# Performance work log

Hardware: AMD Instinct MI355X
Metric: run time of the kernel (lower is better)

The kernel has to match this reference:

```python
import jax, jax.numpy as jnp
import numpy as np

B = 131072
H_DIM = 256
DT = 0.05


def setup_inputs() -> dict:
    key = jax.random.key(0)
    ks = jax.random.split(key, 20)
    w = lambda k, shape, fan_in: jax.random.normal(k, shape, jnp.float32) / np.sqrt(fan_in)
    return {
        "q": jax.random.normal(ks[0], (B, 1), jnp.float32),
        "p": jax.random.normal(ks[1], (B, 1), jnp.float32),
        "u": jax.random.normal(ks[2], (B, 1), jnp.float32),
        "Wk1": w(ks[3], (H_DIM, 2), 2), "bk1": w(ks[4], (H_DIM,), 2),
        "Wk2": w(ks[5], (H_DIM, H_DIM), H_DIM), "bk2": w(ks[6], (H_DIM,), H_DIM),
        "Wk3": w(ks[7], (1, H_DIM), H_DIM), "bk3": w(ks[8], (1,), H_DIM),
        "Wp1": w(ks[9], (H_DIM, 1), 1), "bp1": w(ks[10], (H_DIM,), 1),
        "Wp2": w(ks[11], (H_DIM, H_DIM), H_DIM), "bp2": w(ks[12], (H_DIM,), H_DIM),
        "Wp3": w(ks[13], (1, H_DIM), H_DIM), "bp3": w(ks[14], (1,), H_DIM),
        "b_ctrl": jax.random.normal(ks[15], (1, 1), jnp.float32) * 0.01,
    }


def reference(q, p, u, Wk1, bk1, Wk2, bk2, Wk3, bk3, Wp1, bp1, Wp2, bp2, Wp3, bp3, b_ctrl):
    sp = jax.nn.softplus

    def H(z):  # z: (B, 2) -> (B,)
        qz = z[:, :1]
        hk = sp(z @ Wk1.T + bk1)
        hk = sp(hk @ Wk2.T + bk2)
        T = (hk @ Wk3.T + bk3)[:, 0]
        hp = sp(qz @ Wp1.T + bp1)
        hp = sp(hp @ Wp2.T + bp2)
        V = (hp @ Wp3.T + bp3)[:, 0]
        return T + V

    grad_H = jax.grad(lambda z: H(z).sum())
    # M = J - R with R = 0, J fixed symplectic form
    M = jnp.array([[0.0, 1.0], [-1.0, 0.0]], jnp.float32)
    ctrl = jnp.concatenate([jnp.zeros_like(q), u @ b_ctrl.T], axis=-1)  # (B, 2)

    def dyn(q_, p_):
        # torch detaches z before autograd.grad -> stop_gradient matches semantics
        z = jax.lax.stop_gradient(jnp.concatenate([q_, p_], axis=-1))
        dz = grad_H(z) @ M.T + ctrl
        return dz[:, :1], dz[:, 1:]

    dt = DT
    dq1, dp1 = dyn(q, p)
    dq2, dp2 = dyn(q + 0.5 * dt * dq1, p + 0.5 * dt * dp1)
    dq3, dp3 = dyn(q + 0.5 * dt * dq2, p + 0.5 * dt * dp2)
    dq4, dp4 = dyn(q + dt * dq3, p + dt * dp3)
    q_next = q + dt / 6.0 * (dq1 + 2 * dq2 + 2 * dq3 + dq4)
    p_next = p + dt / 6.0 * (dp1 + 2 * dp2 + 2 * dp3 + dp4)
    return (q_next, p_next)
```

## Files before the change

kernel.cpp:

```cpp
#include <hip/hip_runtime.h>
#include <hip/hip_bf16.h>

#define NB   131072
#define TPB  1024
#define SPB  512

typedef __attribute__((ext_vector_type(8))) short short8;
typedef __attribute__((ext_vector_type(4))) float f32x4;
typedef __attribute__((ext_vector_type(4))) unsigned short ushort4v;

__device__ __forceinline__ unsigned short f2bf(float f) {
    union { float f; unsigned int u; } v; v.f = f;
    unsigned int r = v.u + 0x7fff + ((v.u >> 16) & 1);
    return (unsigned short)(r >> 16);
}

__device__ __forceinline__ unsigned int cvt_pk_bf16(float lo, float hi) {
    unsigned int r;
    asm("v_cvt_pk_bf16_f32 %0, %1, %2" : "=v"(r) : "v"(lo), "v"(hi));
    return r;
}
__device__ __forceinline__ float fexp2(float x) {
    float r; asm("v_exp_f32 %0, %1" : "=v"(r) : "v"(x)); return r;
}
__device__ __forceinline__ float flog2(float x) {
    float r; asm("v_log_f32 %0, %1" : "=v"(r) : "v"(x)); return r;
}

__global__ void prep_weights(const float* __restrict__ Wk2, const float* __restrict__ Wp2,
                             unsigned short* __restrict__ out) {
    int idx = blockIdx.x * blockDim.x + threadIdx.x;
    int n = idx >> 8, k = idx & 255;
    unsigned short a = f2bf(Wk2[idx]);
    out[idx] = a;
    out[65536 + k * 256 + n] = a;
    unsigned short b = f2bf(Wp2[idx]);
    out[131072 + idx] = b;
    out[196608 + k * 256 + n] = b;
}

__launch_bounds__(TPB, 4)
__global__ void phgn_main(const float* __restrict__ q_in, const float* __restrict__ p_in,
                          const float* __restrict__ u_in,
                          const float* __restrict__ Wk1, const float* __restrict__ bk1,
                          const float* __restrict__ bk2, const float* __restrict__ wk3,
                          const float* __restrict__ wp1, const float* __restrict__ bp1,
                          const float* __restrict__ bp2, const float* __restrict__ wp3,
                          const float* __restrict__ bctrl,
                          const unsigned short* __restrict__ Wmats,
                          float* __restrict__ out_q, float* __restrict__ out_p) {
    __shared__ unsigned short bufH0[8192], bufH1[8192];
    __shared__ unsigned short bufG0[8192], bufG1[8192];
    __shared__ float2 qps[SPB];
    __shared__ float2 q0p0[SPB];
    __shared__ float2 accs[SPB];
    __shared__ float  ucs[SPB];
    __shared__ float  slot0[1024], slot1[1024];
    __shared__ float  dHacc[SPB * 2];

    const int tid  = threadIdx.x;
    const int lane = tid & 63;
    const int wave = tid >> 6;
    const int g    = lane >> 4;
    const int l15  = lane & 15;
    const int col  = wave * 16 + l15;
    const int wbase = ((col >> 5) << 9) + (((col >> 3) & 3) << 7) + (col & 7);
    const int hbE = (wave >> 1) * 512 + ((wave & 1) * 2 + (g >> 1)) * 128
                  + l15 * 8 + 4 * (g & 1);
    const int idxLo = ((g << 5) | l15) << 2;
    const int idxHi = idxLo + 64;

    if (tid < SPB) {
        const int sg = blockIdx.x * SPB + tid;
        const float q0 = q_in[sg], p0 = p_in[sg];
        q0p0[tid] = make_float2(q0, p0);
        qps[tid]  = make_float2(q0, p0);
        accs[tid] = make_float2(0.f, 0.f);
        ucs[tid]  = u_in[sg] * bctrl[0];
    }
    __syncthreads();

    const float dt = 0.05f;
    const float LOG2E = 1.44269504f;

    #pragma unroll 1
    for (int st = 0; st < 4; ++st) {
        #pragma unroll 1
        for (int path = 0; path < 2; ++path) {
            const unsigned short* Wf = Wmats + path * 131072;
            const unsigned short* Wb = Wf + 65536;
            const float wq  = (path ? wp1[col] : Wk1[2*col])   * LOG2E;
            const float wp  = (path ? 0.f      : Wk1[2*col+1]) * LOG2E;
            const float b1p = (path ? bp1[col] : bk1[col])     * LOG2E;
            const float w3  =  path ? wp3[col] : wk3[col];
            const float b2p = (path ? bp2[col] : bk2[col])     * LOG2E;

            short8 wfr[8], wbr[8];
            #pragma unroll
            for (int ks = 0; ks < 8; ++ks) {
                wfr[ks] = *(const short8*)(Wf + col * 256 + ks * 32 + g * 8);
                wbr[ks] = *(const short8*)(Wb + col * 256 + ks * 32 + g * 8);
            }

            short8 w1f;
            {
                union { int iv[4]; short8 sv; } uu;
                #pragma unroll
                for (int d = 0; d < 4; ++d) {
                    float lo = 0.f, hi = 0.f;
                    if (g < 2 && l15 < 2) {
                        const int k0 = wave * 16 + g * 8 + 2 * d;
                        if (path == 0) {
                            lo = Wk1[2*k0 + l15];
                            hi = Wk1[2*k0 + 2 + l15];
                        } else if (l15 == 0) {
                            lo = wp1[k0]; hi = wp1[k0 + 1];
                        }
                    }
                    uu.iv[d] = cvt_pk_bf16(lo, hi);
                }
                w1f = uu.sv;
            }

            f32x4 ac, bc;

            auto phA = [&](int pair, unsigned short* HB) {
                const int mb = pair * 32;
                #pragma unroll
                for (int u = 0; u < 2; ++u) {
                    #pragma unroll
                    for (int r = 0; r < 4; r += 2) {
                        const float4 qq = *(const float4*)&qps[mb + u*16 + g*4 + r];
                        const float a0 = fmaf(wq, qq.x, fmaf(wp, qq.y, b1p));
                        const float a1 = fmaf(wq, qq.z, fmaf(wp, qq.w, b1p));
                        const float h0 = flog2(1.0f + fexp2(a0));
                        const float h1 = flog2(1.0f + fexp2(a1));
                        const unsigned int pk = cvt_pk_bf16(h0, h1);
                        HB[u*4096 + wbase + (g*4 + r    ) * 8] = (unsigned short)(pk & 0xffffu);
                        HB[u*4096 + wbase + (g*4 + r + 1) * 8] = (unsigned short)(pk >> 16);
                    }
                }
            };
            auto phB = [&](const unsigned short* HB, int u) {
                ac = (f32x4){0.f, 0.f, 0.f, 0.f};
                #pragma unroll
                for (int ks = 0; ks < 8; ++ks) {
                    const short8 af = *(const short8*)(HB + u*4096 + ks*512 + lane*8);
                    ac = __builtin_amdgcn_mfma_f32_16x16x32_bf16(af, wfr[ks], ac, 0,0,0);
                }
            };
            auto phC = [&](unsigned short* GB, int u) {
                #pragma unroll
                for (int r = 0; r < 4; r += 2) {
                    float gg[2];
                    #pragma unroll
                    for (int v = 0; v < 2; ++v) {
                        const float e = fexp2(ac[r+v] + b2p);
                        gg[v] = w3 * (e * __builtin_amdgcn_rcpf(1.0f + e));
                    }
                    const unsigned int pk = cvt_pk_bf16(gg[0], gg[1]);
                    GB[u*4096 + wbase + (g*4 + r    ) * 8] = (unsigned short)(pk & 0xffffu);
                    GB[u*4096 + wbase + (g*4 + r + 1) * 8] = (unsigned short)(pk >> 16);
                }
            };
            auto phD = [&](const unsigned short* GB, int u) {
                bc = (f32x4){0.f, 0.f, 0.f, 0.f};
                #pragma unroll
                for (int ns = 0; ns < 8; ++ns) {
                    const short8 ag = *(const short8*)(GB + u*4096 + ns*512 + lane*8);
                    bc = __builtin_amdgcn_mfma_f32_16x16x32_bf16(wbr[ns], ag, bc, 0,0,0);
                }
            };
            auto phE = [&](const unsigned short* HB, int u, float* slot) {
                const ushort4v hv = *(const ushort4v*)(HB + u*4096 + hbE);
                float v0, v1, v2, v3;
                {
                    const float h0 = __uint_as_float((unsigned)hv[0] << 16);
                    const float h1 = __uint_as_float((unsigned)hv[1] << 16);
                    const float h2 = __uint_as_float((unsigned)hv[2] << 16);
                    const float h3 = __uint_as_float((unsigned)hv[3] << 16);
                    v0 = bc[0] * (1.0f - fexp2(-h0));
                    v1 = bc[1] * (1.0f - fexp2(-h1));
                    v2 = bc[2] * (1.0f - fexp2(-h2));
                    v3 = bc[3] * (1.0f - fexp2(-h3));
                }
                const int pk01 = (int)cvt_pk_bf16(v0, v1);
                const int pk23 = (int)cvt_pk_bf16(v2, v3);
                union { int iv[4]; short8 sv; } af;
                af.iv[0] = __builtin_amdgcn_ds_bpermute(idxLo, pk01);
                af.iv[1] = __builtin_amdgcn_ds_bpermute(idxLo, pk23);
                af.iv[2] = __builtin_amdgcn_ds_bpermute(idxHi, pk01);
                af.iv[3] = __builtin_amdgcn_ds_bpermute(idxHi, pk23);
                f32x4 dd = (f32x4){0.f, 0.f, 0.f, 0.f};
                dd = __builtin_amdgcn_mfma_f32_16x16x32_bf16(af.sv, w1f, dd, 0,0,0);
                if (l15 < 2) {
                    #pragma unroll
                    for (int r = 0; r < 4; ++r)
                        slot[wave*64 + (u*16 + g*4 + r)*2 + l15] = dd[r];
                }
            };
            auto phF = [&](int pair, const float* slot) {
                if (tid < 64) {
                    const int m2 = tid >> 1, c = tid & 1;
                    if (path == 0 || c == 0) {
                        float s = 0.f;
                        #pragma unroll
                        for (int w = 0; w < 16; ++w) s += slot[w * 64 + tid];
                        const int di = (pair * 32 + m2) * 2 + c;
                        if (path == 0) dHacc[di] = s;
                        else           dHacc[di] += s;
                    }
                }
            };

            phA(0, bufH0);
            __syncthreads();
            phB(bufH0,0); phC(bufG0,0); phB(bufH0,1); phC(bufG0,1);
            phA(1, bufH1);
            __syncthreads();

            #pragma unroll 1
            for (int k2 = 0; k2 < 7; ++k2) {
                const int j = 1 + 2*k2;
                phB(bufH1,0); phD(bufG0,0); phC(bufG1,0); phE(bufH0, 0, slot0);
                phB(bufH1,1); phD(bufG0,1); phC(bufG1,1); phE(bufH0, 1, slot0);
                if (k2) phF(j - 2, slot1);
                phA(j + 1, bufH0);
                __syncthreads();
                phB(bufH0,0); phD(bufG1,0); phC(bufG0,0); phE(bufH1, 0, slot1);
                phB(bufH0,1); phD(bufG1,1); phC(bufG0,1); phE(bufH1, 1, slot1);
                phF(j - 1, slot0);
                phA(j + 2, bufH1);
                __syncthreads();
            }

            phB(bufH1,0); phD(bufG0,0); phC(bufG1,0); phE(bufH0, 0, slot0);
            phB(bufH1,1); phD(bufG0,1); phC(bufG1,1); phE(bufH0, 1, slot0);
            phF(13, slot1);
            __syncthreads();
            phD(bufG1,0); phE(bufH1, 0, slot1);
            phD(bufG1,1); phE(bufH1, 1, slot1);
            phF(14, slot0);
            __syncthreads();
            phF(15, slot1);
            __syncthreads();
        }

        if (tid < SPB) {
            const float dq = dHacc[tid * 2 + 1];
            const float dp = -dHacc[tid * 2 + 0] + ucs[tid];
            const float c = (st == 1 || st == 2) ? 2.f : 1.f;
            float2 acc = accs[tid];
            acc.x += c * dq; acc.y += c * dp;
            accs[tid] = acc;
            if (st < 3) {
                const float hh = (st == 2) ? dt : 0.5f * dt;
                const float2 z0 = q0p0[tid];
                qps[tid] = make_float2(z0.x + hh * dq, z0.y + hh * dp);
            }
        }
        __syncthreads();
    }

    if (tid < SPB) {
        const int sg = blockIdx.x * SPB + tid;
        const float2 z0 = q0p0[tid];
        const float2 acc = accs[tid];
        out_q[sg] = z0.x + (dt / 6.f) * acc.x;
        out_p[sg] = z0.y + (dt / 6.f) * acc.y;
    }
}

extern "C" void kernel_launch(void* const* d_in, const int* in_sizes, int n_in,
                              void* d_out, int out_size, void* d_ws, size_t ws_size,
                              hipStream_t stream) {
    const float* q   = (const float*)d_in[0];
    const float* p   = (const float*)d_in[1];
    const float* u   = (const float*)d_in[2];
    const float* Wk1 = (const float*)d_in[3];
    const float* bk1 = (const float*)d_in[4];
    const float* Wk2 = (const float*)d_in[5];
    const float* bk2 = (const float*)d_in[6];
    const float* Wk3 = (const float*)d_in[7];
    const float* Wp1 = (const float*)d_in[9];
    const float* bp1 = (const float*)d_in[10];
    const float* Wp2 = (const float*)d_in[11];
    const float* bp2 = (const float*)d_in[12];
    const float* Wp3 = (const float*)d_in[13];
    const float* bc  = (const float*)d_in[15];

    unsigned short* wbf = (unsigned short*)d_ws;
    prep_weights<<<256, 256, 0, stream>>>(Wk2, Wp2, wbf);

    float* oq = (float*)d_out;
    phgn_main<<<NB / SPB, TPB, 0, stream>>>(q, p, u, Wk1, bk1, bk2, Wk3, Wp1, bp1, bp2, Wp3,
                                            bc, wbf, oq, oq + NB);
}
```

Before: 424.0 us.

## Fold output weights into backward matrix and remap layer-1 work for packed stores

Pre-multiplies the transposed second-layer weight matrix by the output-layer weights (w3) in the prep kernel, removing a per-element multiply in the sigmoid phase. Layer-1 softplus work is reassigned so each lane computes two adjacent hidden columns and writes packed 32-bit bf16 pairs to LDS instead of separate 16-bit stores. This cuts LDS store instructions and ALU work, at the cost of rounding the w3-scaled product to bf16 rather than scaling in fp32, which changes numerics slightly.

New measurement: 414.4 us. 1.02x faster.

```diff
diff --git a/kernel.cpp b/kernel.cpp
--- a/kernel.cpp
+++ b/kernel.cpp
@@ -28,15 +28,14 @@
 }
 
 __global__ void prep_weights(const float* __restrict__ Wk2, const float* __restrict__ Wp2,
+                             const float* __restrict__ wk3, const float* __restrict__ wp3,
                              unsigned short* __restrict__ out) {
     int idx = blockIdx.x * blockDim.x + threadIdx.x;
     int n = idx >> 8, k = idx & 255;
-    unsigned short a = f2bf(Wk2[idx]);
-    out[idx] = a;
-    out[65536 + k * 256 + n] = a;
-    unsigned short b = f2bf(Wp2[idx]);
-    out[131072 + idx] = b;
-    out[196608 + k * 256 + n] = b;
+    out[idx]                  = f2bf(Wk2[idx]);
+    out[65536 + k * 256 + n]  = f2bf(Wk2[idx] * wk3[n]);
+    out[131072 + idx]         = f2bf(Wp2[idx]);
+    out[196608 + k * 256 + n] = f2bf(Wp2[idx] * wp3[n]);
 }
 
 __launch_bounds__(TPB, 4)
@@ -65,6 +64,12 @@
     const int l15  = lane & 15;
     const int col  = wave * 16 + l15;
     const int wbase = ((col >> 5) << 9) + (((col >> 3) & 3) << 7) + (col & 7);
+    const int t8  = l15 & 7;
+    const int rg  = g * 2 + (l15 >> 3);
+    const int uA  = rg >> 2;
+    const int r0A = (rg & 3) * 4;
+    const int c0  = wave * 16 + 2 * t8;
+    const int wbA = uA * 4096 + ((c0 >> 5) << 9) + (((c0 >> 3) & 3) << 7) + (c0 & 7);
     const int hbE = (wave >> 1) * 512 + ((wave & 1) * 2 + (g >> 1)) * 128
                   + l15 * 8 + 4 * (g & 1);
     const int idxLo = ((g << 5) | l15) << 2;
@@ -89,11 +94,21 @@
         for (int path = 0; path < 2; ++path) {
             const unsigned short* Wf = Wmats + path * 131072;
             const unsigned short* Wb = Wf + 65536;
-            const float wq  = (path ? wp1[col] : Wk1[2*col])   * LOG2E;
-            const float wp  = (path ? 0.f      : Wk1[2*col+1]) * LOG2E;
-            const float b1p = (path ? bp1[col] : bk1[col])     * LOG2E;
-            const float w3  =  path ? wp3[col] : wk3[col];
-            const float b2p = (path ? bp2[col] : bk2[col])     * LOG2E;
+            float wqA0, wpA0, b1A0, wqA1, wpA1, b1A1;
+            if (path == 0) {
+                const float4 wv = *(const float4*)(Wk1 + 2 * c0);
+                wqA0 = wv.x * LOG2E; wpA0 = wv.y * LOG2E;
+                wqA1 = wv.z * LOG2E; wpA1 = wv.w * LOG2E;
+                const float2 bv = *(const float2*)(bk1 + c0);
+                b1A0 = bv.x * LOG2E; b1A1 = bv.y * LOG2E;
+            } else {
+                const float2 wv = *(const float2*)(wp1 + c0);
+                wqA0 = wv.x * LOG2E; wqA1 = wv.y * LOG2E;
+                wpA0 = 0.f; wpA1 = 0.f;
+                const float2 bv = *(const float2*)(bp1 + c0);
+                b1A0 = bv.x * LOG2E; b1A1 = bv.y * LOG2E;
+            }
+            const float b2p = (path ? bp2[col] : bk2[col]) * LOG2E;
 
             short8 wfr[8], wbr[8];
             #pragma unroll
@@ -125,20 +140,20 @@
             f32x4 ac, bc;
 
             auto phA = [&](int pair, unsigned short* HB) {
-                const int mb = pair * 32;
-                #pragma unroll
-                for (int u = 0; u < 2; ++u) {
-                    #pragma unroll
-                    for (int r = 0; r < 4; r += 2) {
-                        const float4 qq = *(const float4*)&qps[mb + u*16 + g*4 + r];
-                        const float a0 = fmaf(wq, qq.x, fmaf(wp, qq.y, b1p));
-                        const float a1 = fmaf(wq, qq.z, fmaf(wp, qq.w, b1p));
-                        const float h0 = flog2(1.0f + fexp2(a0));
-                        const float h1 = flog2(1.0f + fexp2(a1));
-                        const unsigned int pk = cvt_pk_bf16(h0, h1);
-                        HB[u*4096 + wbase + (g*4 + r    ) * 8] = (unsigned short)(pk & 0xffffu);
-                        HB[u*4096 + wbase + (g*4 + r + 1) * 8] = (unsigned short)(pk >> 16);
-                    }
+                const int mb = pair * 32 + uA * 16 + r0A;
+                #pragma unroll
+                for (int i = 0; i < 4; i += 2) {
+                    const float4 q2 = *(const float4*)&qps[mb + i];
+                    const float a00 = fmaf(wqA0, q2.x, fmaf(wpA0, q2.y, b1A0));
+                    const float a01 = fmaf(wqA1, q2.x, fmaf(wpA1, q2.y, b1A1));
+                    const float a10 = fmaf(wqA0, q2.z, fmaf(wpA0, q2.w, b1A0));
+                    const float a11 = fmaf(wqA1, q2.z, fmaf(wpA1, q2.w, b1A1));
+                    const float h00 = flog2(1.0f + fexp2(a00));
+                    const float h01 = flog2(1.0f + fexp2(a01));
+                    const float h10 = flog2(1.0f + fexp2(a10));
+                    const float h11 = flog2(1.0f + fexp2(a11));
+                    *(unsigned int*)(HB + wbA + (r0A + i    ) * 8) = cvt_pk_bf16(h00, h01);
+                    *(unsigned int*)(HB + wbA + (r0A + i + 1) * 8) = cvt_pk_bf16(h10, h11);
                 }
             };
             auto phB = [&](const unsigned short* HB, int u) {
@@ -156,7 +171,7 @@
                     #pragma unroll
                     for (int v = 0; v < 2; ++v) {
                         const float e = fexp2(ac[r+v] + b2p);
-                        gg[v] = w3 * (e * __builtin_amdgcn_rcpf(1.0f + e));
+                        gg[v] = e * __builtin_amdgcn_rcpf(1.0f + e);
                     }
                     const unsigned int pk = cvt_pk_bf16(gg[0], gg[1]);
                     GB[u*4096 + wbase + (g*4 + r    ) * 8] = (unsigned short)(pk & 0xffffu);
@@ -290,7 +305,7 @@
     const float* bc  = (const float*)d_in[15];
 
     unsigned short* wbf = (unsigned short*)d_ws;
-    prep_weights<<<256, 256, 0, stream>>>(Wk2, Wp2, wbf);
+    prep_weights<<<256, 256, 0, stream>>>(Wk2, Wp2, Wk3, Wp3, wbf);
 
     float* oq = (float*)d_out;
     phgn_main<<<NB / SPB, TPB, 0, stream>>>(q, p, u, Wk1, bk1, bk2, Wk3, Wp1, bp1, bp2, Wp3,
```
